# Kernel optimization log

Measured on AMD Instinct MI355X. Metric: run time of the kernel, lower is better.

Reference implementation:

```python
import jax, jax.numpy as jnp
import numpy as np
import math

D_MODEL = 512
N_HEADS = 16
HEAD_DIM = D_MODEL // N_HEADS  # 32
ROPE_BASE = 10000.0
B, T = 2, 2048


def build_rope_cache(seq_len, dim, base):
    inv_freq = 1.0 / (base ** (jnp.arange(0, dim, 2, dtype=jnp.float32) / dim))  # (dim/2,)
    t = jnp.arange(seq_len, dtype=jnp.float32)
    freqs = jnp.outer(t, inv_freq)                  # (T, dim/2)
    emb = jnp.concatenate([freqs, freqs], axis=-1)  # (T, dim)
    return jnp.cos(emb), jnp.sin(emb)


def rotate_half(x):
    x1, x2 = jnp.split(x, 2, axis=-1)
    return jnp.concatenate([-x2, x1], axis=-1)


def apply_rope(x, cos, sin):
    # x: (B,H,T,hd); cos/sin: (T,hd) broadcast over B,H
    return x * cos + rotate_half(x) * sin


def setup_inputs() -> dict:
    key = jax.random.key(0)
    k1, k2, k3 = jax.random.split(key, 3)
    x = jax.random.normal(k1, (B, T, D_MODEL), dtype=jnp.float32)
    w_qkv = jax.random.normal(k2, (3 * D_MODEL, D_MODEL), dtype=jnp.float32) * 0.02
    w_o = jax.random.normal(k3, (D_MODEL, D_MODEL), dtype=jnp.float32) * 0.02
    return {"x": x, "w_qkv": w_qkv, "w_o": w_o}


def reference(x, w_qkv, w_o):
    Bx, Tx, C = x.shape
    H, hd = N_HEADS, HEAD_DIM
    qkv = x @ w_qkv.T                                   # (B,T,3C)
    qkv = qkv.reshape(Bx, Tx, 3, H, hd).transpose(0, 2, 3, 1, 4)  # (B,3,H,T,hd)
    q, k, v = qkv[:, 0], qkv[:, 1], qkv[:, 2]
    cos, sin = build_rope_cache(Tx, hd, ROPE_BASE)
    q = apply_rope(q, cos, sin)
    k = apply_rope(k, cos, sin)
    scale = 1.0 / math.sqrt(hd)
    scores = jnp.einsum('bhqd,bhkd->bhqk', q, k) * scale  # (B,H,T,T)
    causal = jnp.tril(jnp.ones((Tx, Tx), dtype=bool))
    scores = jnp.where(causal, scores, jnp.finfo(scores.dtype).min)
    attn = jax.nn.softmax(scores, axis=-1)
    out = jnp.einsum('bhqk,bhkd->bhqd', attn, v)          # (B,H,T,hd)
    out = out.transpose(0, 2, 1, 3).reshape(Bx, Tx, C)    # (B,T,C)
    return out @ w_o.T
```

## Files before the change

### kernel.cpp

```cpp
#include <hip/hip_runtime.h>
#include <hip/hip_bf16.h>
#include <math.h>

#define D_MODEL 512
#define N_HEADS 16
#define HEAD_DIM 32
#define T_SEQ 2048
#define B_SZ 2
#define NTOK (B_SZ * T_SEQ)
#define QKV_DIM (3 * D_MODEL)

typedef short short8 __attribute__((ext_vector_type(8)));
typedef float f32x4  __attribute__((ext_vector_type(4)));

__device__ __forceinline__ float bf2f(unsigned int u16) {
    union { unsigned int i; float f; } v;
    v.i = u16 << 16;
    return v.f;
}

__device__ __forceinline__ unsigned short f2bf(float f) {
    union { float f; unsigned int i; } v;
    v.f = f;
    unsigned int lsb = (v.i >> 16) & 1u;
    v.i += 0x7fffu + lsb;
    return (unsigned short)(v.i >> 16);
}

__device__ __forceinline__ unsigned int f2bf_tru32(float f) {
    union { float f; unsigned int i; } v;
    v.f = f;
    return v.i >> 16;
}

__device__ __forceinline__ void gld_lds16(const void* g, void* l) {
    __builtin_amdgcn_global_load_lds(
        (const __attribute__((address_space(1))) void*)g,
        (__attribute__((address_space(3))) void*)l, 16, 0, 0);
}

#define N4_X   (NTOK * D_MODEL / 4)
#define N4_WQ  (QKV_DIM * D_MODEL / 4)
#define N4_WO  (D_MODEL * D_MODEL / 4)
__global__ __launch_bounds__(256) void cvt_all(const float* __restrict__ x,
                                               const float* __restrict__ wq,
                                               const float* __restrict__ wo,
                                               unsigned short* __restrict__ xb,
                                               unsigned short* __restrict__ wqb,
                                               unsigned short* __restrict__ wob) {
    int i = blockIdx.x * 256 + threadIdx.x;
    const float* in;
    unsigned short* out;
    int k;
    if (i < N4_X)                { in = x;  out = xb;  k = i; }
    else if (i < N4_X + N4_WQ)   { in = wq; out = wqb; k = i - N4_X; }
    else if (i < N4_X + N4_WQ + N4_WO) { in = wo; out = wob; k = i - N4_X - N4_WQ; }
    else return;
    float4 v = ((const float4*)in)[k];
    ushort4 o;
    o.x = f2bf(v.x); o.y = f2bf(v.y); o.z = f2bf(v.z); o.w = f2bf(v.w);
    ((ushort4*)out)[k] = o;
}

#define LOG2_10000_D16 0.8304820237218405f
#define QSCALE_LOG2 0.2550348788f

template<int MT, int LDA, int LDC, bool OUT_BF16, bool ROPE>
__global__ __launch_bounds__(256) void gemm_nt(const unsigned short* __restrict__ A,
                                               const unsigned short* __restrict__ B,
                                               void* __restrict__ Cout,
                                               unsigned short* __restrict__ kb,
                                               unsigned short* __restrict__ vt) {
    __shared__ unsigned short Als[MT * 64];
    __shared__ unsigned short Bls[64 * 64];

    const int tid = threadIdx.x;
    const int m0 = blockIdx.y * MT;
    const int n0 = blockIdx.x * 64;

    const int wid  = tid >> 6;
    const int lane = tid & 63;
    const int c    = lane & 15;
    const int quad = lane >> 4;
    const int wm = (wid >> 1) * (MT / 2);
    const int wn = (wid & 1) * 32;
    const int MI = MT / 32;

    f32x4 acc[MI][2];
#pragma unroll
    for (int i = 0; i < MI; ++i)
#pragma unroll
        for (int j = 0; j < 2; ++j) acc[i][j] = (f32x4)0.f;

    const int srow = wid * 8 + (lane >> 3);
    const int schk = lane & 7;

    for (int k0 = 0; k0 < 512; k0 += 64) {
#pragma unroll
        for (int it = 0; it < MT / 32; ++it) {
            const unsigned short* g = A + (size_t)(m0 + it * 32 + srow) * LDA + k0 + schk * 8;
            gld_lds16(g, &Als[(it * 32 + srow) * 64 + schk * 8]);
        }
#pragma unroll
        for (int it = 0; it < 2; ++it) {
            const unsigned short* g = B + (size_t)(n0 + it * 32 + srow) * 512 + k0 + schk * 8;
            gld_lds16(g, &Bls[(it * 32 + srow) * 64 + schk * 8]);
        }
        __syncthreads();

#pragma unroll
        for (int kk = 0; kk < 2; ++kk) {
            short8 af[MI], bfr[2];
#pragma unroll
            for (int i = 0; i < MI; ++i)
                af[i] = *(const short8*)&Als[(wm + i * 16 + c) * 64 + kk * 32 + quad * 8];
#pragma unroll
            for (int j = 0; j < 2; ++j)
                bfr[j] = *(const short8*)&Bls[(wn + j * 16 + c) * 64 + kk * 32 + quad * 8];
#pragma unroll
            for (int i = 0; i < MI; ++i)
#pragma unroll
                for (int j = 0; j < 2; ++j)
                    acc[i][j] = __builtin_amdgcn_mfma_f32_16x16x32_bf16(af[i], bfr[j], acc[i][j], 0, 0, 0);
        }
        __syncthreads();
    }

    if (ROPE) {
        const int sec = n0 >> 9;
        if (sec == 0) {
            const float invf = exp2f(-LOG2_10000_D16 * (float)c);
#pragma unroll
            for (int i = 0; i < MI; ++i)
#pragma unroll
                for (int r = 0; r < 4; ++r) {
                    int t = (m0 + wm + i * 16 + quad * 4 + r) & (T_SEQ - 1);
                    float ss, cc;
                    sincosf((float)t * invf, &ss, &cc);
                    float e0 = acc[i][0][r], e1 = acc[i][1][r];
                    acc[i][0][r] = (e0 * cc - e1 * ss) * QSCALE_LOG2;
                    acc[i][1][r] = (e1 * cc + e0 * ss) * QSCALE_LOG2;
                }
        } else if (sec == 1) {
            const float invf = exp2f(-LOG2_10000_D16 * (float)c);
            const int head = ((n0 - 512) + wn) >> 5;
#pragma unroll
            for (int i = 0; i < MI; ++i)
#pragma unroll
                for (int r = 0; r < 4; ++r) {
                    int mm = m0 + wm + i * 16 + quad * 4 + r;
                    int t = mm & (T_SEQ - 1);
                    float ss, cc;
                    sincosf((float)t * invf, &ss, &cc);
                    float e0 = acc[i][0][r], e1 = acc[i][1][r];
                    float k0v = e0 * cc - e1 * ss;
                    float k1v = e1 * cc + e0 * ss;
                    int bh = (mm >> 11) * 16 + head;
                    int s = (t & 3) ^ ((t >> 2) & 3);
                    unsigned short* row = kb + ((size_t)(bh * 2048 + t)) * 32;
                    row[((((c) >> 3) ^ s) << 3) + (c & 7)]        = f2bf(k0v);
                    row[((((16 + c) >> 3) ^ s) << 3) + (c & 7)]   = f2bf(k1v);
                }
            return;
        } else {
#pragma unroll
            for (int i = 0; i < MI; ++i)
#pragma unroll
                for (int j = 0; j < 2; ++j) {
                    int nl = n0 - 1024 + wn + j * 16;
                    int head = nl >> 5;
                    int d = (nl & 16) + c;
                    int mm = m0 + wm + i * 16 + quad * 4;
                    int bI = mm >> 11;
                    int pos = mm & (T_SEQ - 1);
                    int phys = ((pos >> 3) & 7) ^ (d & 7);
                    size_t base = ((size_t)((bI * 16 + head) * 32 + d)) * 2048
                                  + (pos & ~63) + (phys << 3) + (pos & 7);
                    ushort4 st;
                    st.x = f2bf(acc[i][j][0]); st.y = f2bf(acc[i][j][1]);
                    st.z = f2bf(acc[i][j][2]); st.w = f2bf(acc[i][j][3]);
                    *(ushort4*)(vt + base) = st;
                }
            return;
        }
    }

    if (OUT_BF16) {
        unsigned short* Cb = (unsigned short*)Cout;
#pragma unroll
        for (int i = 0; i < MI; ++i)
#pragma unroll
            for (int j = 0; j < 2; ++j)
#pragma unroll
                for (int r = 0; r < 4; ++r) {
                    int mm = m0 + wm + i * 16 + quad * 4 + r;
                    int nn = n0 + wn + j * 16 + c;
                    Cb[(size_t)mm * LDC + nn] = f2bf(acc[i][j][r]);
                }
    } else {
        float* Cf = (float*)Cout;
#pragma unroll
        for (int i = 0; i < MI; ++i)
#pragma unroll
            for (int j = 0; j < 2; ++j)
#pragma unroll
                for (int r = 0; r < 4; ++r) {
                    int mm = m0 + wm + i * 16 + quad * 4 + r;
                    int nn = n0 + wn + j * 16 + c;
                    Cf[(size_t)mm * LDC + nn] = acc[i][j][r];
                }
    }
}

__global__ __launch_bounds__(256) void flash_attn(const unsigned short* __restrict__ qb,
                                                  const unsigned short* __restrict__ kb,
                                                  const unsigned short* __restrict__ vt,
                                                  unsigned short* __restrict__ ob) {
    __shared__ unsigned short KtL[64 * 32];
    __shared__ unsigned short VtL[32 * 64];
    __shared__ unsigned short Pl[4 * 16 * 72];

    const int idx   = blockIdx.x;
    const int qtile = 31 - (idx >> 5);
    const int bh    = idx & 31;
    const int b = bh >> 4, h = bh & 15;
    const int tid  = threadIdx.x;
    const int wid  = tid >> 6;
    const int lane = tid & 63;
    const int c    = lane & 15;
    const int quad = lane >> 4;

    const int q0w = qtile * 64 + wid * 16;
    const int sK = (c & 3) ^ ((c >> 2) & 3);
    const int sP = c & 7;

    short8 qf = *(const short8*)(qb + ((size_t)(b * T_SEQ + q0w + c)) * 512 + h * HEAD_DIM + quad * 8);

    f32x4 accO[2];
    accO[0] = (f32x4)0.f; accO[1] = (f32x4)0.f;
    float l_part = 0.f;

    unsigned short* plw = &Pl[wid * 16 * 72];

    const int krow = tid >> 2, kch = tid & 3;
    const int vd   = tid >> 3, vch = tid & 7;
    const unsigned short* kbase = kb + (size_t)bh * 2048 * 32 + (size_t)krow * 32 + kch * 8;
    const unsigned short* vbase = vt + ((size_t)(bh * 32 + vd)) * 2048 + vch * 8;

    uint4 kreg = *(const uint4*)(kbase);
    uint4 vreg = *(const uint4*)(vbase);

    const int nkt = qtile + 1;
    for (int kt = 0; kt < nkt; ++kt) {
        __syncthreads();
        *(uint4*)&KtL[tid * 8] = kreg;
        *(uint4*)&VtL[tid * 8] = vreg;
        __syncthreads();

        if (kt + 1 < nkt) {
            kreg = *(const uint4*)(kbase + (size_t)(kt + 1) * 64 * 32);
            vreg = *(const uint4*)(vbase + (kt + 1) * 64);
        }

        f32x4 sv[4];
#pragma unroll
        for (int j = 0; j < 4; ++j) {
            short8 kf = *(const short8*)&KtL[(j * 16 + c) * 32 + ((quad ^ sK) << 3)];
            f32x4 z = (f32x4)0.f;
            sv[j] = __builtin_amdgcn_mfma_f32_16x16x32_bf16(kf, qf, z, 0, 0, 0);
        }

        if (kt == qtile) {
#pragma unroll
            for (int j = 0; j < 4; ++j)
#pragma unroll
                for (int r = 0; r < 4; ++r)
                    if (j * 16 + quad * 4 + r > wid * 16 + c) sv[j][r] = -30000.f;
        }

#pragma unroll
        for (int j = 0; j < 4; ++j) {
            float p0 = exp2f(sv[j][0]);
            float p1 = exp2f(sv[j][1]);
            float p2 = exp2f(sv[j][2]);
            float p3 = exp2f(sv[j][3]);
            l_part += (p0 + p1) + (p2 + p3);
            unsigned int w0 = f2bf_tru32(p0) | (f2bf_tru32(p1) << 16);
            unsigned int w1 = f2bf_tru32(p2) | (f2bf_tru32(p3) << 16);
            uint2 w = make_uint2(w0, w1);
            *(uint2*)&plw[c * 72 + j * 16 + quad * 4] = w;
        }

#pragma unroll
        for (int kk = 0; kk < 2; ++kk) {
            short8 pf = *(const short8*)&plw[c * 72 + kk * 32 + quad * 8];
#pragma unroll
            for (int ns = 0; ns < 2; ++ns) {
                short8 vf = *(const short8*)&VtL[(ns * 16 + c) * 64 + (((kk * 4 + quad) ^ sP) << 3)];
                accO[ns] = __builtin_amdgcn_mfma_f32_16x16x32_bf16(pf, vf, accO[ns], 0, 0, 0);
            }
        }
    }

    float lr = l_part;
    lr += __shfl_xor(lr, 16);
    lr += __shfl_xor(lr, 32);
#pragma unroll
    for (int r = 0; r < 4; ++r) {
        float lq = __shfl(lr, quad * 4 + r);
        float inv = 1.f / lq;
        int qg = q0w + quad * 4 + r;
        unsigned short* op = ob + ((size_t)(b * T_SEQ + qg)) * 512 + h * HEAD_DIM;
#pragma unroll
        for (int ns = 0; ns < 2; ++ns)
            op[ns * 16 + c] = f2bf(accO[ns][r] * inv);
    }
}

extern "C" void kernel_launch(void* const* d_in, const int* in_sizes, int n_in,
                              void* d_out, int out_size, void* d_ws, size_t ws_size,
                              hipStream_t stream) {
    const float* x     = (const float*)d_in[0];
    const float* w_qkv = (const float*)d_in[1];
    const float* w_o   = (const float*)d_in[2];
    float* out = (float*)d_out;

    unsigned short* qb  = (unsigned short*)d_ws;
    unsigned short* kb  = qb  + (size_t)NTOK * D_MODEL;
    unsigned short* vt  = kb  + (size_t)32 * 2048 * 32;
    unsigned short* xb  = vt  + (size_t)32 * 32 * 2048;
    unsigned short* wqb = xb  + (size_t)NTOK * D_MODEL;
    unsigned short* wob = wqb + (size_t)QKV_DIM * D_MODEL;
    unsigned short* ob  = wob + (size_t)D_MODEL * D_MODEL;

    {
        int total = N4_X + N4_WQ + N4_WO;
        cvt_all<<<(total + 255) / 256, 256, 0, stream>>>(x, w_qkv, w_o, xb, wqb, wob);
    }
    {
        dim3 grid(QKV_DIM / 64, NTOK / 128);
        gemm_nt<128, D_MODEL, D_MODEL, true, true><<<grid, 256, 0, stream>>>(xb, wqb, qb, kb, vt);
    }
    {
        flash_attn<<<1024, 256, 0, stream>>>(qb, kb, vt, ob);
    }
    {
        dim3 grid(D_MODEL / 64, NTOK / 64);
        gemm_nt<64, D_MODEL, D_MODEL, false, false><<<grid, 256, 0, stream>>>(ob, wob, out, nullptr, nullptr);
    }
}
```

Before: 119.5 us.

## Load K/V MFMA fragments directly from global memory, dropping LDS staging

The attention kernel no longer stages K and V tiles through shared memory with block-wide barriers. Each wave loads its own K and V MFMA fragments straight from global memory into registers and prefetches the next tile's fragments. The QKV projection epilogue now writes K and V in plain unswizzled layouts to match. This removes two __syncthreads per key tile and the LDS round trip. In exchange, each of the four waves loads the same K/V data separately, so global/L2 traffic per block goes up, and register pressure rises.

Measured after the change: 147.8 us. 1.24x slower.

```diff
diff --git a/kernel.cpp b/kernel.cpp
--- a/kernel.cpp
+++ b/kernel.cpp
@@ -156,10 +156,9 @@
                     float k0v = e0 * cc - e1 * ss;
                     float k1v = e1 * cc + e0 * ss;
                     int bh = (mm >> 11) * 16 + head;
-                    int s = (t & 3) ^ ((t >> 2) & 3);
                     unsigned short* row = kb + ((size_t)(bh * 2048 + t)) * 32;
-                    row[((((c) >> 3) ^ s) << 3) + (c & 7)]        = f2bf(k0v);
-                    row[((((16 + c) >> 3) ^ s) << 3) + (c & 7)]   = f2bf(k1v);
+                    row[c]      = f2bf(k0v);
+                    row[16 + c] = f2bf(k1v);
                 }
             return;
         } else {
@@ -173,9 +172,7 @@
                     int mm = m0 + wm + i * 16 + quad * 4;
                     int bI = mm >> 11;
                     int pos = mm & (T_SEQ - 1);
-                    int phys = ((pos >> 3) & 7) ^ (d & 7);
-                    size_t base = ((size_t)((bI * 16 + head) * 32 + d)) * 2048
-                                  + (pos & ~63) + (phys << 3) + (pos & 7);
+                    size_t base = ((size_t)((bI * 16 + head) * 32 + d)) * 2048 + pos;
                     ushort4 st;
                     st.x = f2bf(acc[i][j][0]); st.y = f2bf(acc[i][j][1]);
                     st.z = f2bf(acc[i][j][2]); st.w = f2bf(acc[i][j][3]);
@@ -216,8 +213,6 @@
                                                   const unsigned short* __restrict__ kb,
                                                   const unsigned short* __restrict__ vt,
                                                   unsigned short* __restrict__ ob) {
-    __shared__ unsigned short KtL[64 * 32];
-    __shared__ unsigned short VtL[32 * 64];
     __shared__ unsigned short Pl[4 * 16 * 72];
 
     const int idx   = blockIdx.x;
@@ -231,8 +226,6 @@
     const int quad = lane >> 4;
 
     const int q0w = qtile * 64 + wid * 16;
-    const int sK = (c & 3) ^ ((c >> 2) & 3);
-    const int sP = c & 7;
 
     short8 qf = *(const short8*)(qb + ((size_t)(b * T_SEQ + q0w + c)) * 512 + h * HEAD_DIM + quad * 8);
 
@@ -242,32 +235,32 @@
 
     unsigned short* plw = &Pl[wid * 16 * 72];
 
-    const int krow = tid >> 2, kch = tid & 3;
-    const int vd   = tid >> 3, vch = tid & 7;
-    const unsigned short* kbase = kb + (size_t)bh * 2048 * 32 + (size_t)krow * 32 + kch * 8;
-    const unsigned short* vbase = vt + ((size_t)(bh * 32 + vd)) * 2048 + vch * 8;
-
-    uint4 kreg = *(const uint4*)(kbase);
-    uint4 vreg = *(const uint4*)(vbase);
+    const unsigned short* kB = kb + (size_t)bh * 2048 * 32;
+    const unsigned short* vB = vt + (size_t)bh * 32 * 2048;
 
     const int nkt = qtile + 1;
+
+    short8 kf[4], vf[4];
+#pragma unroll
+    for (int j = 0; j < 4; ++j)
+        kf[j] = *(const short8*)(kB + (size_t)(j * 16 + c) * 32 + quad * 8);
+#pragma unroll
+    for (int u = 0; u < 4; ++u)
+        vf[u] = *(const short8*)(vB + (size_t)(((u & 1) * 16 + c)) * 2048 + (u >> 1) * 32 + quad * 8);
+
     for (int kt = 0; kt < nkt; ++kt) {
-        __syncthreads();
-        *(uint4*)&KtL[tid * 8] = kreg;
-        *(uint4*)&VtL[tid * 8] = vreg;
-        __syncthreads();
+        f32x4 sv[4];
+#pragma unroll
+        for (int j = 0; j < 4; ++j) {
+            f32x4 z = (f32x4)0.f;
+            sv[j] = __builtin_amdgcn_mfma_f32_16x16x32_bf16(kf[j], qf, z, 0, 0, 0);
+        }
 
         if (kt + 1 < nkt) {
-            kreg = *(const uint4*)(kbase + (size_t)(kt + 1) * 64 * 32);
-            vreg = *(const uint4*)(vbase + (kt + 1) * 64);
-        }
-
-        f32x4 sv[4];
-#pragma unroll
-        for (int j = 0; j < 4; ++j) {
-            short8 kf = *(const short8*)&KtL[(j * 16 + c) * 32 + ((quad ^ sK) << 3)];
-            f32x4 z = (f32x4)0.f;
-            sv[j] = __builtin_amdgcn_mfma_f32_16x16x32_bf16(kf, qf, z, 0, 0, 0);
+            const unsigned short* kN = kB + (size_t)(kt + 1) * 64 * 32;
+#pragma unroll
+            for (int j = 0; j < 4; ++j)
+                kf[j] = *(const short8*)(kN + (size_t)(j * 16 + c) * 32 + quad * 8);
         }
 
         if (kt == qtile) {
@@ -295,10 +288,15 @@
         for (int kk = 0; kk < 2; ++kk) {
             short8 pf = *(const short8*)&plw[c * 72 + kk * 32 + quad * 8];
 #pragma unroll
-            for (int ns = 0; ns < 2; ++ns) {
-                short8 vf = *(const short8*)&VtL[(ns * 16 + c) * 64 + (((kk * 4 + quad) ^ sP) << 3)];
-                accO[ns] = __builtin_amdgcn_mfma_f32_16x16x32_bf16(pf, vf, accO[ns], 0, 0, 0);
-            }
+            for (int ns = 0; ns < 2; ++ns)
+                accO[ns] = __builtin_amdgcn_mfma_f32_16x16x32_bf16(pf, vf[kk * 2 + ns], accO[ns], 0, 0, 0);
+        }
+
+        if (kt + 1 < nkt) {
+#pragma unroll
+            for (int u = 0; u < 4; ++u)
+                vf[u] = *(const short8*)(vB + (size_t)(((u & 1) * 16 + c)) * 2048
+                                         + (kt + 1) * 64 + (u >> 1) * 32 + quad * 8);
         }
     }
 
```
